# Performance work log

Measured on AMD Instinct MI355X. Metric: run time of the kernel, lower is better.

## Reference

```python
import jax, jax.numpy as jnp
import numpy as np

CENTER_LR = 0.5  # default center_lr in _compute_centroids_mb


def setup_inputs() -> dict:
    key = jax.random.key(0)
    k1, k2, k3 = jax.random.split(key, 3)
    N, D, K = 16384, 1024, 1024
    embedded = jax.random.normal(k1, (N, D), dtype=jnp.float32)
    centers = jax.random.normal(k2, (K, D), dtype=jnp.float32)
    count = jax.random.randint(k3, (K,), 0, 10000, dtype=jnp.int32)
    return {"embedded": embedded, "centers": centers, "count": count}


def _sq_euclidean(x, c):
    # ||x - c||^2 via expansion; avoids materializing [N, K, D]
    x2 = jnp.sum(x * x, axis=1, keepdims=True)        # [N, 1]
    c2 = jnp.sum(c * c, axis=1)[None, :]              # [1, K]
    d = x2 + c2 - 2.0 * (x @ c.T)                     # [N, K]
    return jnp.maximum(d, 0.0)


def reference(embedded, centers, count):
    N, D = embedded.shape
    K = centers.shape[0]
    # predict_hard: argmin of squared euclidean distance
    dist = _sq_euclidean(embedded, centers)           # [N, K]
    labels = jnp.argmin(dist, axis=1)                 # [N]
    # _int_to_one_hot assignment matrix
    A = jax.nn.one_hot(labels, K, dtype=embedded.dtype)  # [N, K]
    # segmented reduction: batch_cluster_sums[k] = sum_{i: label_i=k} embedded[i]
    # (embedded is detached in the original -> stop_gradient)
    batch_cluster_sums = jnp.einsum('nk,nd->kd', A, jax.lax.stop_gradient(embedded))  # [K, D]
    mask_sum = jnp.sum(A, axis=0)                     # [K]
    nonzero = mask_sum != 0                           # [K]
    # count EMA (only for clusters present in the batch)
    cc = count.astype(jnp.float32)
    cc_new = jnp.where(nonzero, (1.0 - CENTER_LR) * cc + CENTER_LR * mask_sum, cc)
    per_center_lr = 1.0 / (cc_new + 1.0)              # [K]
    batch_centers = batch_cluster_sums / jnp.where(nonzero, mask_sum, 1.0)[:, None]
    new_centers = jnp.where(
        nonzero[:, None],
        (1.0 - per_center_lr)[:, None] * centers + per_center_lr[:, None] * batch_centers,
        centers,
    )
    return new_centers
```

## Files before the change

kernel.cpp:

```cpp
#include <hip/hip_runtime.h>

typedef __attribute__((ext_vector_type(8))) short bf16x8;
typedef __attribute__((ext_vector_type(4))) float f32x4;

__device__ __forceinline__ unsigned short f2bf(float f) {
    unsigned u = __float_as_uint(f);
    unsigned r = (u + 0x7FFFu + ((u >> 16) & 1u)) >> 16;
    return (unsigned short)r;
}

__device__ __forceinline__ void gload16(const unsigned short* g, unsigned short* l) {
    __builtin_amdgcn_global_load_lds((const __attribute__((address_space(1))) void*)g,
                                     (__attribute__((address_space(3))) void*)l, 16, 0, 0);
}

#define SCHED0() __builtin_amdgcn_sched_barrier(0)
#define BAR2()   do { SCHED0(); __builtin_amdgcn_s_barrier(); SCHED0(); } while (0)


__global__ void conv_x_kernel(const float* __restrict__ x, unsigned short* __restrict__ xb, int total8) {
    int i = blockIdx.x * blockDim.x + threadIdx.x;
    if (i >= total8) return;
    const float4* xv = (const float4*)x;
    float4 a = xv[(size_t)i * 2];
    float4 b = xv[(size_t)i * 2 + 1];
    uint4 o;
    o.x = (unsigned)f2bf(a.x) | ((unsigned)f2bf(a.y) << 16);
    o.y = (unsigned)f2bf(a.z) | ((unsigned)f2bf(a.w) << 16);
    o.z = (unsigned)f2bf(b.x) | ((unsigned)f2bf(b.y) << 16);
    o.w = (unsigned)f2bf(b.z) | ((unsigned)f2bf(b.w) << 16);
    ((uint4*)xb)[i] = o;
}

__global__ void conv_c_kernel(const float* __restrict__ c, unsigned short* __restrict__ cb,
                              float* __restrict__ c2, int D) {
    int k = blockIdx.x;
    int tid = threadIdx.x;
    const float4 v = ((const float4*)(c + (long)k * D))[tid];
    uint2 o;
    o.x = (unsigned)f2bf(v.x) | ((unsigned)f2bf(v.y) << 16);
    o.y = (unsigned)f2bf(v.z) | ((unsigned)f2bf(v.w) << 16);
    ((uint2*)(cb + (long)k * D))[tid] = o;
    float s = v.x * v.x + v.y * v.y + v.z * v.z + v.w * v.w;
    #pragma unroll
    for (int d = 1; d < 64; d <<= 1) s += __shfl_xor(s, d, 64);
    __shared__ float wsum[4];
    int lane = tid & 63, w = tid >> 6;
    if (lane == 0) wsum[w] = s;
    __syncthreads();
    if (tid == 0) c2[k] = wsum[0] + wsum[1] + wsum[2] + wsum[3];
}

__global__ void init_packed_kernel(unsigned long long* __restrict__ p, int n) {
    int i = blockIdx.x * blockDim.x + threadIdx.x;
    if (i < n) p[i] = ~0ull;
}

__global__ void __launch_bounds__(512, 2)
gemm_argmin_kernel(const unsigned short* __restrict__ Xb,
                   const unsigned short* __restrict__ Cb,
                   const float* __restrict__ c2,
                   unsigned long long* __restrict__ packed,
                   int D, int nt) {
    __shared__ unsigned short sh[65536];
    const int tid  = threadIdx.x;
    const int lane = tid & 63;
    const int w    = tid >> 6;
    const int wr   = w >> 2;
    const int wc   = w & 3;
    const long rowbase = (long)blockIdx.x * 256;
    const int  colbase = blockIdx.y * 256;

    const int fr = lane & 15;
    const int g  = lane >> 4;
    const int f7 = fr & 7;
    const int q0 = g ^ f7;
    const int q1 = (4 + g) ^ f7;
    const int abase0 = (wr * 128 + fr) * 64;
    const int bbase0 = 32768 + (wc * 64 + fr) * 64;

    f32x4 acc[8][4] = {};
    bf16x8 a[4][2], b[4][2];

    auto stageA = [&](int kt, int buf) {
        unsigned short* base = sh + buf * 16384;
        const unsigned short* gsrc = Xb + rowbase * D + kt * 64;
        #pragma unroll
        for (int j = 0; j < 4; ++j) {
            int c = j * 512 + w * 64 + lane;
            int r = c >> 3;
            int q = (c & 7) ^ (r & 7);
            gload16(gsrc + (long)r * D + q * 8, base + (j * 512 + w * 64) * 8);
        }
    };
    auto stageB = [&](int kt, int buf) {
        unsigned short* base = sh + 32768 + buf * 16384;
        const unsigned short* gsrc = Cb + (long)colbase * D + kt * 64;
        #pragma unroll
        for (int j = 0; j < 4; ++j) {
            int c = j * 512 + w * 64 + lane;
            int r = c >> 3;
            int q = (c & 7) ^ (r & 7);
            gload16(gsrc + (long)r * D + q * 8, base + (j * 512 + w * 64) * 8);
        }
    };

    stageA(0, 0);
    stageB(0, 0);
    if (nt > 1) stageA(1, 1);
    asm volatile("s_waitcnt vmcnt(4)" ::: "memory");
    BAR2();

    for (int t = 0; t < nt; ++t) {
        const int buf = t & 1;
        const int ab = abase0 + buf * 16384;
        const int bb = bbase0 + buf * 16384;

        #pragma unroll
        for (int m = 0; m < 4; ++m) {
            a[m][0] = *(const bf16x8*)&sh[ab + m * 1024 + q0 * 8];
            a[m][1] = *(const bf16x8*)&sh[ab + m * 1024 + q1 * 8];
        }
        #pragma unroll
        for (int n = 0; n < 2; ++n) {
            b[n][0] = *(const bf16x8*)&sh[bb + n * 1024 + q0 * 8];
            b[n][1] = *(const bf16x8*)&sh[bb + n * 1024 + q1 * 8];
        }
        if (t < nt - 1) stageB(t + 1, buf ^ 1);
        BAR2();
        __builtin_amdgcn_s_setprio(1);
        #pragma unroll
        for (int m = 0; m < 4; ++m)
            #pragma unroll
            for (int n = 0; n < 2; ++n) {
                acc[m][n] = __builtin_amdgcn_mfma_f32_16x16x32_bf16(a[m][0], b[n][0], acc[m][n], 0, 0, 0);
                acc[m][n] = __builtin_amdgcn_mfma_f32_16x16x32_bf16(a[m][1], b[n][1], acc[m][n], 0, 0, 0);
            }
        __builtin_amdgcn_s_setprio(0);
        BAR2();

        #pragma unroll
        for (int n = 2; n < 4; ++n) {
            b[n][0] = *(const bf16x8*)&sh[bb + n * 1024 + q0 * 8];
            b[n][1] = *(const bf16x8*)&sh[bb + n * 1024 + q1 * 8];
        }
        BAR2();
        __builtin_amdgcn_s_setprio(1);
        #pragma unroll
        for (int m = 0; m < 4; ++m)
            #pragma unroll
            for (int n = 2; n < 4; ++n) {
                acc[m][n] = __builtin_amdgcn_mfma_f32_16x16x32_bf16(a[m][0], b[n][0], acc[m][n], 0, 0, 0);
                acc[m][n] = __builtin_amdgcn_mfma_f32_16x16x32_bf16(a[m][1], b[n][1], acc[m][n], 0, 0, 0);
            }
        __builtin_amdgcn_s_setprio(0);
        BAR2();

        #pragma unroll
        for (int m = 0; m < 4; ++m) {
            a[m][0] = *(const bf16x8*)&sh[ab + (m + 4) * 1024 + q0 * 8];
            a[m][1] = *(const bf16x8*)&sh[ab + (m + 4) * 1024 + q1 * 8];
        }
        BAR2();
        __builtin_amdgcn_s_setprio(1);
        #pragma unroll
        for (int m = 0; m < 4; ++m)
            #pragma unroll
            for (int n = 0; n < 2; ++n) {
                acc[m + 4][n] = __builtin_amdgcn_mfma_f32_16x16x32_bf16(a[m][0], b[n][0], acc[m + 4][n], 0, 0, 0);
                acc[m + 4][n] = __builtin_amdgcn_mfma_f32_16x16x32_bf16(a[m][1], b[n][1], acc[m + 4][n], 0, 0, 0);
            }
        __builtin_amdgcn_s_setprio(0);
        BAR2();

        if (t < nt - 2) {
            stageA(t + 2, buf);
            asm volatile("s_waitcnt vmcnt(4)" ::: "memory");
        } else if (t == nt - 2) {
            asm volatile("s_waitcnt vmcnt(0)" ::: "memory");
        }
        BAR2();
        __builtin_amdgcn_s_setprio(1);
        #pragma unroll
        for (int m = 0; m < 4; ++m)
            #pragma unroll
            for (int n = 2; n < 4; ++n) {
                acc[m + 4][n] = __builtin_amdgcn_mfma_f32_16x16x32_bf16(a[m][0], b[n][0], acc[m + 4][n], 0, 0, 0);
                acc[m + 4][n] = __builtin_amdgcn_mfma_f32_16x16x32_bf16(a[m][1], b[n][1], acc[m + 4][n], 0, 0, 0);
            }
        __builtin_amdgcn_s_setprio(0);
        BAR2();
    }

    float c2v[4];
    int   kcol[4];
    #pragma unroll
    for (int n = 0; n < 4; ++n) {
        kcol[n] = colbase + wc * 64 + n * 16 + fr;
        c2v[n]  = c2[kcol[n]];
    }
    #pragma unroll
    for (int m = 0; m < 8; ++m) {
        #pragma unroll
        for (int reg = 0; reg < 4; ++reg) {
            unsigned long long best = ~0ull;
            #pragma unroll
            for (int n = 0; n < 4; ++n) {
                float score = c2v[n] - 2.0f * acc[m][n][reg];
                unsigned u = __float_as_uint(score);
                u ^= (u >> 31) ? 0xFFFFFFFFu : 0x80000000u;
                unsigned long long cand = ((unsigned long long)u << 32) | (unsigned)kcol[n];
                best = cand < best ? cand : best;
            }
            #pragma unroll
            for (int s = 1; s < 16; s <<= 1) {
                unsigned long long other = __shfl_xor(best, s, 64);
                best = other < best ? other : best;
            }
            if (fr == 0) {
                long row = rowbase + wr * 128 + m * 16 + g * 4 + reg;
                atomicMin(&packed[row], best);
            }
        }
    }
}

__global__ void segsum_partial_kernel(const unsigned long long* __restrict__ packed,
                                      const float* __restrict__ emb,
                                      float* __restrict__ partial,
                                      int* __restrict__ pcount,
                                      int N, int D) {
    const int k   = blockIdx.x;
    const int s   = blockIdx.y;
    const int tid = threadIdx.x;
    const int grp = tid >> 8;
    const int ct  = tid & 255;
    const int lane = tid & 63, w = tid >> 6;

    __shared__ int idxbuf[2048];
    __shared__ int cnts[16];
    __shared__ float4 red[4][256];

    const int slice = N >> 3;
    const int base0 = s * slice;
    int total = 0;
    for (int base = base0; base < base0 + slice; base += 1024) {
        const int n = base + tid;
        const bool m = ((unsigned)(packed[n] & 0xFFFFFFFFull) == (unsigned)k);
        const unsigned long long bal = __ballot(m);
        if (lane == 0) cnts[w] = (int)__popcll(bal);
        __syncthreads();
        int myoff = total, run = total;
        #pragma unroll
        for (int w2 = 0; w2 < 16; ++w2) {
            if (w2 == w) myoff = run;
            run += cnts[w2];
        }
        if (m) idxbuf[myoff + (int)__popcll(bal & ((1ull << lane) - 1ull))] = n;
        total = run;
        __syncthreads();
    }

    float4 acc = {0.f, 0.f, 0.f, 0.f};
    for (int j = grp; j < total; j += 4) {
        const int row = idxbuf[j];
        const float4 v = *(const float4*)(emb + (long)row * D + ct * 4);
        acc.x += v.x; acc.y += v.y; acc.z += v.z; acc.w += v.w;
    }
    red[grp][ct] = acc;
    __syncthreads();
    if (grp == 0) {
        float4 r = red[0][ct];
        #pragma unroll
        for (int q = 1; q < 4; ++q) {
            const float4 v = red[q][ct];
            r.x += v.x; r.y += v.y; r.z += v.z; r.w += v.w;
        }
        *(float4*)(partial + ((long)(k * 8 + s)) * D + ct * 4) = r;
    }
    if (tid == 0) pcount[k * 8 + s] = total;
}

__global__ void finalize_kernel(const float* __restrict__ partial,
                                const int* __restrict__ pcount,
                                const float* __restrict__ centers,
                                const int* __restrict__ cnt,
                                float* __restrict__ out, int D) {
    const int k = blockIdx.x;
    const int ct = threadIdx.x;
    float4 acc = {0.f, 0.f, 0.f, 0.f};
    int mtot = 0;
    #pragma unroll
    for (int s = 0; s < 8; ++s) {
        const float4 p = *(const float4*)(partial + ((long)(k * 8 + s)) * D + ct * 4);
        acc.x += p.x; acc.y += p.y; acc.z += p.z; acc.w += p.w;
        mtot += pcount[k * 8 + s];
    }
    const float4 cv = *(const float4*)(centers + (long)k * D + ct * 4);
    float4 o;
    if (mtot > 0) {
        float ccn = 0.5f * (float)cnt[k] + 0.5f * (float)mtot;
        float lr  = 1.0f / (ccn + 1.0f);
        float im  = 1.0f / (float)mtot;
        float om  = 1.0f - lr;
        o.x = om * cv.x + lr * (acc.x * im);
        o.y = om * cv.y + lr * (acc.y * im);
        o.z = om * cv.z + lr * (acc.z * im);
        o.w = om * cv.w + lr * (acc.w * im);
    } else {
        o = cv;
    }
    *(float4*)(out + (long)k * D + ct * 4) = o;
}


extern "C" void kernel_launch(void* const* d_in, const int* in_sizes, int n_in,
                              void* d_out, int out_size, void* d_ws, size_t ws_size,
                              hipStream_t stream) {
    const float* emb = (const float*)d_in[0];
    const float* cen = (const float*)d_in[1];
    const int*   cnt = (const int*)d_in[2];
    float* out = (float*)d_out;
    const int K = in_sizes[2];
    const int D = in_sizes[1] / K;
    const int N = in_sizes[0] / D;

    char* ws = (char*)d_ws;
    size_t xb_bytes = (size_t)N * D * 2;
    size_t cb_bytes = (size_t)K * D * 2;
    unsigned short* Xb = (unsigned short*)ws;
    unsigned short* Cb = (unsigned short*)(ws + xb_bytes);
    float* c2 = (float*)(ws + xb_bytes + cb_bytes);
    unsigned long long* packed = (unsigned long long*)(ws + xb_bytes + cb_bytes + (size_t)K * 4);
    float* partial = (float*)ws;
    int* pcount = (int*)(ws + xb_bytes + cb_bytes + (size_t)K * 4 + (size_t)N * 8);

    int total8 = N * D / 8;
    conv_x_kernel<<<dim3((total8 + 255) / 256), dim3(256), 0, stream>>>(emb, Xb, total8);
    conv_c_kernel<<<dim3(K), dim3(256), 0, stream>>>(cen, Cb, c2, D);
    init_packed_kernel<<<dim3((N + 255) / 256), dim3(256), 0, stream>>>(packed, N);
    gemm_argmin_kernel<<<dim3(N / 256, K / 256), dim3(512), 0, stream>>>(Xb, Cb, c2, packed, D, D / 64);
    segsum_partial_kernel<<<dim3(K, 8), dim3(1024), 0, stream>>>(packed, emb, partial, pcount, N, D);
    finalize_kernel<<<dim3(K), dim3(256), 0, stream>>>(partial, pcount, cen, cnt, out, D);
}
```

Baseline: 107.0 us.

## Restage GEMM prefetch with fewer barriers, compact labels, and halve segsum split

The GEMM main loop now prefetches both A and B for the next k-tile at the start of each iteration. It waits with vmcnt(0) before the last MFMA group and drops several block-wide barriers, loading the first B fragments of the next tile early. The packed-label init is folded into the centers conversion kernel, removing a launch. A small kernel extracts 16-bit labels so the segmented-sum kernel scans 2-byte labels instead of 8-byte packed values, and the segsum split over N is reduced from 8 to 4 slices. The trade-off is that A is now prefetched only one tile ahead instead of two, which may expose more load latency, and there is one extra launch for label extraction.

```diff
diff --git a/kernel.cpp b/kernel.cpp
--- a/kernel.cpp
+++ b/kernel.cpp
@@ -14,8 +14,7 @@
                                      (__attribute__((address_space(3))) void*)l, 16, 0, 0);
 }
 
-#define SCHED0() __builtin_amdgcn_sched_barrier(0)
-#define BAR2()   do { SCHED0(); __builtin_amdgcn_s_barrier(); SCHED0(); } while (0)
+#define BARRIER() do { asm volatile("" ::: "memory"); __builtin_amdgcn_s_barrier(); asm volatile("" ::: "memory"); } while (0)
 
 
 __global__ void conv_x_kernel(const float* __restrict__ x, unsigned short* __restrict__ xb, int total8) {
@@ -33,7 +32,8 @@
 }
 
 __global__ void conv_c_kernel(const float* __restrict__ c, unsigned short* __restrict__ cb,
-                              float* __restrict__ c2, int D) {
+                              float* __restrict__ c2, unsigned long long* __restrict__ packed,
+                              int N, int D) {
     int k = blockIdx.x;
     int tid = threadIdx.x;
     const float4 v = ((const float4*)(c + (long)k * D))[tid];
@@ -49,11 +49,8 @@
     if (lane == 0) wsum[w] = s;
     __syncthreads();
     if (tid == 0) c2[k] = wsum[0] + wsum[1] + wsum[2] + wsum[3];
-}
-
-__global__ void init_packed_kernel(unsigned long long* __restrict__ p, int n) {
-    int i = blockIdx.x * blockDim.x + threadIdx.x;
-    if (i < n) p[i] = ~0ull;
+    int gid = k * 256 + tid;
+    if (gid < N) packed[gid] = ~0ull;
 }
 
 __global__ void __launch_bounds__(512, 2)
@@ -107,14 +104,25 @@
 
     stageA(0, 0);
     stageB(0, 0);
-    if (nt > 1) stageA(1, 1);
-    asm volatile("s_waitcnt vmcnt(4)" ::: "memory");
-    BAR2();
+    asm volatile("s_waitcnt vmcnt(0)" ::: "memory");
+    BARRIER();
+    {
+        const int bb = bbase0;
+        #pragma unroll
+        for (int n = 0; n < 2; ++n) {
+            b[n][0] = *(const bf16x8*)&sh[bb + n * 1024 + q0 * 8];
+            b[n][1] = *(const bf16x8*)&sh[bb + n * 1024 + q1 * 8];
+        }
+    }
 
     for (int t = 0; t < nt; ++t) {
-        const int buf = t & 1;
-        const int ab = abase0 + buf * 16384;
-        const int bb = bbase0 + buf * 16384;
+        const int p  = t & 1;
+        const int ab = abase0 + p * 16384;
+        const int bb = bbase0 + p * 16384;
+        const int bbn = bbase0 + (p ^ 1) * 16384;
+
+        if (t < nt - 1) { stageA(t + 1, p ^ 1); stageB(t + 1, p ^ 1); }
+        BARRIER();
 
         #pragma unroll
         for (int m = 0; m < 4; ++m) {
@@ -122,12 +130,10 @@
             a[m][1] = *(const bf16x8*)&sh[ab + m * 1024 + q1 * 8];
         }
         #pragma unroll
-        for (int n = 0; n < 2; ++n) {
+        for (int n = 2; n < 4; ++n) {
             b[n][0] = *(const bf16x8*)&sh[bb + n * 1024 + q0 * 8];
             b[n][1] = *(const bf16x8*)&sh[bb + n * 1024 + q1 * 8];
         }
-        if (t < nt - 1) stageB(t + 1, buf ^ 1);
-        BAR2();
         __builtin_amdgcn_s_setprio(1);
         #pragma unroll
         for (int m = 0; m < 4; ++m)
@@ -137,14 +143,8 @@
                 acc[m][n] = __builtin_amdgcn_mfma_f32_16x16x32_bf16(a[m][1], b[n][1], acc[m][n], 0, 0, 0);
             }
         __builtin_amdgcn_s_setprio(0);
-        BAR2();
-
-        #pragma unroll
-        for (int n = 2; n < 4; ++n) {
-            b[n][0] = *(const bf16x8*)&sh[bb + n * 1024 + q0 * 8];
-            b[n][1] = *(const bf16x8*)&sh[bb + n * 1024 + q1 * 8];
-        }
-        BAR2();
+        BARRIER();
+
         __builtin_amdgcn_s_setprio(1);
         #pragma unroll
         for (int m = 0; m < 4; ++m)
@@ -154,14 +154,13 @@
                 acc[m][n] = __builtin_amdgcn_mfma_f32_16x16x32_bf16(a[m][1], b[n][1], acc[m][n], 0, 0, 0);
             }
         __builtin_amdgcn_s_setprio(0);
-        BAR2();
+        BARRIER();
 
         #pragma unroll
         for (int m = 0; m < 4; ++m) {
             a[m][0] = *(const bf16x8*)&sh[ab + (m + 4) * 1024 + q0 * 8];
             a[m][1] = *(const bf16x8*)&sh[ab + (m + 4) * 1024 + q1 * 8];
         }
-        BAR2();
         __builtin_amdgcn_s_setprio(1);
         #pragma unroll
         for (int m = 0; m < 4; ++m)
@@ -171,15 +170,16 @@
                 acc[m + 4][n] = __builtin_amdgcn_mfma_f32_16x16x32_bf16(a[m][1], b[n][1], acc[m + 4][n], 0, 0, 0);
             }
         __builtin_amdgcn_s_setprio(0);
-        BAR2();
-
-        if (t < nt - 2) {
-            stageA(t + 2, buf);
-            asm volatile("s_waitcnt vmcnt(4)" ::: "memory");
-        } else if (t == nt - 2) {
-            asm volatile("s_waitcnt vmcnt(0)" ::: "memory");
-        }
-        BAR2();
+        if (t < nt - 1) asm volatile("s_waitcnt vmcnt(0)" ::: "memory");
+        BARRIER();
+
+        if (t < nt - 1) {
+            #pragma unroll
+            for (int n = 0; n < 2; ++n) {
+                b[n][0] = *(const bf16x8*)&sh[bbn + n * 1024 + q0 * 8];
+                b[n][1] = *(const bf16x8*)&sh[bbn + n * 1024 + q1 * 8];
+            }
+        }
         __builtin_amdgcn_s_setprio(1);
         #pragma unroll
         for (int m = 0; m < 4; ++m)
@@ -189,7 +189,6 @@
                 acc[m + 4][n] = __builtin_amdgcn_mfma_f32_16x16x32_bf16(a[m][1], b[n][1], acc[m + 4][n], 0, 0, 0);
             }
         __builtin_amdgcn_s_setprio(0);
-        BAR2();
     }
 
     float c2v[4];
@@ -225,7 +224,13 @@
     }
 }
 
-__global__ void segsum_partial_kernel(const unsigned long long* __restrict__ packed,
+__global__ void extract16_kernel(const unsigned long long* __restrict__ p,
+                                 unsigned short* __restrict__ lab, int n) {
+    int i = blockIdx.x * blockDim.x + threadIdx.x;
+    if (i < n) lab[i] = (unsigned short)(p[i] & 0xFFFFull);
+}
+
+__global__ void segsum_partial_kernel(const unsigned short* __restrict__ lab,
                                       const float* __restrict__ emb,
                                       float* __restrict__ partial,
                                       int* __restrict__ pcount,
@@ -237,16 +242,16 @@
     const int ct  = tid & 255;
     const int lane = tid & 63, w = tid >> 6;
 
-    __shared__ int idxbuf[2048];
+    __shared__ int idxbuf[4096];
     __shared__ int cnts[16];
     __shared__ float4 red[4][256];
 
-    const int slice = N >> 3;
+    const int slice = N >> 2;
     const int base0 = s * slice;
     int total = 0;
     for (int base = base0; base < base0 + slice; base += 1024) {
         const int n = base + tid;
-        const bool m = ((unsigned)(packed[n] & 0xFFFFFFFFull) == (unsigned)k);
+        const bool m = (lab[n] == (unsigned short)k);
         const unsigned long long bal = __ballot(m);
         if (lane == 0) cnts[w] = (int)__popcll(bal);
         __syncthreads();
@@ -276,9 +281,9 @@
             const float4 v = red[q][ct];
             r.x += v.x; r.y += v.y; r.z += v.z; r.w += v.w;
         }
-        *(float4*)(partial + ((long)(k * 8 + s)) * D + ct * 4) = r;
-    }
-    if (tid == 0) pcount[k * 8 + s] = total;
+        *(float4*)(partial + ((long)(k * 4 + s)) * D + ct * 4) = r;
+    }
+    if (tid == 0) pcount[k * 4 + s] = total;
 }
 
 __global__ void finalize_kernel(const float* __restrict__ partial,
@@ -291,10 +296,10 @@
     float4 acc = {0.f, 0.f, 0.f, 0.f};
     int mtot = 0;
     #pragma unroll
-    for (int s = 0; s < 8; ++s) {
-        const float4 p = *(const float4*)(partial + ((long)(k * 8 + s)) * D + ct * 4);
+    for (int s = 0; s < 4; ++s) {
+        const float4 p = *(const float4*)(partial + ((long)(k * 4 + s)) * D + ct * 4);
         acc.x += p.x; acc.y += p.y; acc.z += p.z; acc.w += p.w;
-        mtot += pcount[k * 8 + s];
+        mtot += pcount[k * 4 + s];
     }
     const float4 cv = *(const float4*)(centers + (long)k * D + ct * 4);
     float4 o;
@@ -332,14 +337,15 @@
     unsigned short* Cb = (unsigned short*)(ws + xb_bytes);
     float* c2 = (float*)(ws + xb_bytes + cb_bytes);
     unsigned long long* packed = (unsigned long long*)(ws + xb_bytes + cb_bytes + (size_t)K * 4);
+    unsigned short* lab16 = (unsigned short*)(ws + xb_bytes + cb_bytes + (size_t)K * 4 + (size_t)N * 8);
+    int* pcount = (int*)(ws + xb_bytes + cb_bytes + (size_t)K * 4 + (size_t)N * 8 + (size_t)N * 2);
     float* partial = (float*)ws;
-    int* pcount = (int*)(ws + xb_bytes + cb_bytes + (size_t)K * 4 + (size_t)N * 8);
 
     int total8 = N * D / 8;
     conv_x_kernel<<<dim3((total8 + 255) / 256), dim3(256), 0, stream>>>(emb, Xb, total8);
-    conv_c_kernel<<<dim3(K), dim3(256), 0, stream>>>(cen, Cb, c2, D);
-    init_packed_kernel<<<dim3((N + 255) / 256), dim3(256), 0, stream>>>(packed, N);
+    conv_c_kernel<<<dim3(K), dim3(256), 0, stream>>>(cen, Cb, c2, packed, N, D);
     gemm_argmin_kernel<<<dim3(N / 256, K / 256), dim3(512), 0, stream>>>(Xb, Cb, c2, packed, D, D / 64);
-    segsum_partial_kernel<<<dim3(K, 8), dim3(1024), 0, stream>>>(packed, emb, partial, pcount, N, D);
+    extract16_kernel<<<dim3((N + 255) / 256), dim3(256), 0, stream>>>(packed, lab16, N);
+    segsum_partial_kernel<<<dim3(K, 4), dim3(1024), 0, stream>>>(lab16, emb, partial, pcount, N, D);
     finalize_kernel<<<dim3(K), dim3(256), 0, stream>>>(partial, pcount, cen, cnt, out, D);
 }
```

After: 101.1 us. -5.6%, faster.
